# Kernel tuning notes

Hardware: AMD Instinct MI355X
Metric: run time of the kernel (lower is better)

Reference implementation:

```python
import jax, jax.numpy as jnp
import numpy as np

B, H, S, D = 8, 12, 1024, 64

def setup_inputs() -> dict:
    key = jax.random.key(0)
    kq, kk, kv = jax.random.split(key, 3)
    q = jax.random.normal(kq, (B, H, S, D), dtype=jnp.float32)
    k = jax.random.normal(kk, (B, H, S, D), dtype=jnp.float32)
    v = jax.random.normal(kv, (B, H, S, D), dtype=jnp.float32)
    scale = 8  # sqrt(d_head)
    return {"q": q, "k": k, "v": v, "scale": scale}

def reference(q, k, v, scale):
    # scores: (B,H,S,S) = q @ k^T / scale, softmax over last axis
    scores = jnp.einsum('bhqd,bhkd->bhqk', q, k) / scale
    attention_score = jax.nn.softmax(scores, axis=-1)
    # context: (B,H,S,D)
    attention_context = jnp.einsum('bhqk,bhkd->bhqd', attention_score, v)
    return (attention_score, attention_context)
```

## Files before the change

kernel.cpp:

```cpp
#include <hip/hip_runtime.h>


#define SLEN 1024
#define DHEAD 64
#define NBH 96
#define QROWS 16

typedef __attribute__((ext_vector_type(4))) float f32x4;
typedef __attribute__((ext_vector_type(8))) __bf16 bf16x8;

#define PL_STRIDE 1032

struct SMem {
  __bf16 pl[QROWS][PL_STRIDE];
  __bf16 qt[QROWS][72];
  float red[8][QROWS];
  float mrow[QROWS];
  float invrow[QROWS];
  float ctxr[4][64][4];
};

__global__ __launch_bounds__(512, 4)
void attn_fused(const float* __restrict__ Qp, const float* __restrict__ Kp,
                const float* __restrict__ Vp, const int* __restrict__ scale_p,
                float* __restrict__ out) {
  __shared__ SMem sm;
  const int tid  = threadIdx.x;
  const int w    = tid >> 6;
  const int lane = tid & 63;
  const int quad = lane >> 4;
  const int c16  = lane & 15;

  const int bid  = blockIdx.x;
  const int xcd  = bid & 7;
  const int slot = bid >> 3;
  const int bh   = xcd * 12 + (slot >> 6);
  const int qbase = (slot & 63) * QROWS;

  int siv = *scale_p;
  float fs = (siv >= 1 && siv <= (1 << 24)) ? (float)siv : __int_as_float(siv);
  const float inv_scale = 1.0f / fs;

  const float* Qg = Qp + ((size_t)bh * SLEN + qbase) * DHEAD;
  const float* Kg = Kp + (size_t)bh * SLEN * DHEAD;
  const float* Vg = Vp + (size_t)bh * SLEN * DHEAD;

  if (tid < 256) {
    int r = tid >> 4, d = (tid & 15) * 4;
    f32x4 qv = *(const f32x4*)(Qg + (size_t)r * DHEAD + d);
    #pragma unroll
    for (int j = 0; j < 4; ++j) sm.qt[r][d + j] = (__bf16)(qv[j] * inv_scale);
  }
  __syncthreads();

  bf16x8 af[2];
  #pragma unroll
  for (int k0 = 0; k0 < 2; ++k0)
    af[k0] = *(const bf16x8*)&sm.qt[c16][k0 * 32 + quad * 8];

  f32x4 acc[8];
  {
    f32x4 z = {0.0f, 0.0f, 0.0f, 0.0f};
    #pragma unroll
    for (int ct = 0; ct < 8; ++ct) acc[ct] = z;
  }

  #pragma unroll
  for (int ct = 0; ct < 8; ++ct) {
    int krow = w * 128 + ct * 16 + c16;
    const float* kr = Kg + (size_t)krow * DHEAD + quad * 8;
    f32x4 k0a = *(const f32x4*)(kr);
    f32x4 k0b = *(const f32x4*)(kr + 4);
    f32x4 k1a = *(const f32x4*)(kr + 32);
    f32x4 k1b = *(const f32x4*)(kr + 36);
    bf16x8 b0, b1;
    #pragma unroll
    for (int j = 0; j < 4; ++j) {
      b0[j]     = (__bf16)k0a[j];
      b0[j + 4] = (__bf16)k0b[j];
      b1[j]     = (__bf16)k1a[j];
      b1[j + 4] = (__bf16)k1b[j];
    }
    acc[ct] = __builtin_amdgcn_mfma_f32_16x16x32_bf16(af[0], b0, acc[ct], 0, 0, 0);
    acc[ct] = __builtin_amdgcn_mfma_f32_16x16x32_bf16(af[1], b1, acc[ct], 0, 0, 0);
  }

  float mx[4];
  #pragma unroll
  for (int i = 0; i < 4; ++i) {
    float m = acc[0][i];
    #pragma unroll
    for (int ct = 1; ct < 8; ++ct) m = fmaxf(m, acc[ct][i]);
    mx[i] = m;
  }
  #pragma unroll
  for (int off = 1; off < 16; off <<= 1)
    #pragma unroll
    for (int i = 0; i < 4; ++i)
      mx[i] = fmaxf(mx[i], __shfl_xor(mx[i], off));
  if (c16 == 0) {
    #pragma unroll
    for (int i = 0; i < 4; ++i) sm.red[w][quad * 4 + i] = mx[i];
  }
  __syncthreads();
  if (tid < QROWS) {
    float m = sm.red[0][tid];
    #pragma unroll
    for (int w2 = 1; w2 < 8; ++w2) m = fmaxf(m, sm.red[w2][tid]);
    sm.mrow[tid] = m;
  }
  __syncthreads();

  float sum4[4];
  #pragma unroll
  for (int i = 0; i < 4; ++i) {
    float m = sm.mrow[quad * 4 + i];
    float s = 0.0f;
    #pragma unroll
    for (int ct = 0; ct < 8; ++ct) {
      float e = __expf(acc[ct][i] - m);
      acc[ct][i] = e;
      s += e;
    }
    sum4[i] = s;
  }
  #pragma unroll
  for (int off = 1; off < 16; off <<= 1)
    #pragma unroll
    for (int i = 0; i < 4; ++i)
      sum4[i] += __shfl_xor(sum4[i], off);
  if (c16 == 0) {
    #pragma unroll
    for (int i = 0; i < 4; ++i) sm.red[w][quad * 4 + i] = sum4[i];
  }
  __syncthreads();
  if (tid < QROWS) {
    float s = 0.0f;
    #pragma unroll
    for (int w2 = 0; w2 < 8; ++w2) s += sm.red[w2][tid];
    sm.invrow[tid] = 1.0f / s;
  }
  __syncthreads();

  #pragma unroll
  for (int i = 0; i < 4; ++i) {
    int row = quad * 4 + i;
    float inv = sm.invrow[row];
    bf16x8 pk;
    #pragma unroll
    for (int ct = 0; ct < 8; ++ct) {
      float p = acc[ct][i] * inv;
      acc[ct][i] = p;
      pk[ct] = (__bf16)p;
    }
    *(bf16x8*)&sm.pl[row][w * 128 + c16 * 8] = pk;
  }
  __syncthreads();

  const int kpar = w >> 2;
  const int dt   = w & 3;
  const float* Vb = Vg + dt * 16 + c16;

  f32x4 ctx = {0.0f, 0.0f, 0.0f, 0.0f};
  float vr0[8], vr1[8];
  bf16x8 pa0, pa1;

  auto ldv = [&](float (&dst)[8], int itl) {
    int kb = (kpar * 4 + (itl >> 2)) * 128 + (itl & 3) * 4 + quad;
    #pragma unroll
    for (int j = 0; j < 8; ++j)
      dst[j] = Vb[(size_t)((kb + j * 16) * DHEAD)];
  };
  auto lda = [&](bf16x8& d, int itl) {
    d = *(const bf16x8*)&sm.pl[c16][(kpar * 4 + (itl >> 2)) * 128 +
                                    (itl & 3) * 32 + quad * 8];
  };

  ldv(vr0, 0); lda(pa0, 0);
  #pragma unroll
  for (int it = 0; it < 16; it += 2) {
    ldv(vr1, it + 1); lda(pa1, it + 1);
    bf16x8 bf0;
    #pragma unroll
    for (int j = 0; j < 8; ++j) bf0[j] = (__bf16)vr0[j];
    ctx = __builtin_amdgcn_mfma_f32_16x16x32_bf16(pa0, bf0, ctx, 0, 0, 0);
    if (it + 2 < 16) { ldv(vr0, it + 2); lda(pa0, it + 2); }
    bf16x8 bf1;
    #pragma unroll
    for (int j = 0; j < 8; ++j) bf1[j] = (__bf16)vr1[j];
    ctx = __builtin_amdgcn_mfma_f32_16x16x32_bf16(pa1, bf1, ctx, 0, 0, 0);
  }

  if (kpar == 1) *(f32x4*)&sm.ctxr[dt][lane][0] = ctx;
  __syncthreads();
  if (kpar == 0) {
    f32x4 o = *(const f32x4*)&sm.ctxr[dt][lane][0];
    float* outC = out + (size_t)NBH * SLEN * SLEN;
    #pragma unroll
    for (int i = 0; i < 4; ++i) {
      float r = ctx[i] + o[i];
      outC[((size_t)bh * SLEN + qbase + quad * 4 + i) * DHEAD + dt * 16 + c16] = r;
    }
  }

  #pragma unroll
  for (int i = 0; i < 4; ++i) {
    int row = quad * 4 + i;
    float* orow = out + ((size_t)bh * SLEN + qbase + row) * SLEN;
    #pragma unroll
    for (int ct = 0; ct < 8; ++ct)
      orow[w * 128 + ct * 16 + c16] = acc[ct][i];
  }
}

extern "C" void kernel_launch(void* const* d_in, const int* in_sizes, int n_in,
                              void* d_out, int out_size, void* d_ws, size_t ws_size,
                              hipStream_t stream) {
  (void)in_sizes; (void)n_in; (void)d_ws; (void)ws_size; (void)out_size;
  const float* q = (const float*)d_in[0];
  const float* k = (const float*)d_in[1];
  const float* v = (const float*)d_in[2];
  const int* scale = (const int*)d_in[3];
  float* out = (float*)d_out;
  dim3 grid((SLEN / QROWS) * NBH);
  dim3 block(512);
  hipLaunchKernelGGL(attn_fused, grid, block, 0, stream, q, k, v, scale, out);
}
```

Before: 693.5 us.

## Pre-convert K and transposed V to bf16 in workspace, restructure main kernel

Adds a prepass kernel that converts K to bf16 and V to a transposed bf16 layout in the workspace, so the main kernel reads half the bytes and gets contiguous V loads instead of strided scalar gathers. The main kernel drops to 256 threads with 4 waves each covering 256 keys. It computes K·Q^T so each lane owns a query column, writes the probabilities directly as f32x4 from registers without the LDS P buffer, and reduces partial contexts through LDS. It costs an extra launch and a workspace round-trip per call, and falls back to an unstaged path when the workspace is too small.

```diff
diff --git a/kernel.cpp b/kernel.cpp
--- a/kernel.cpp
+++ b/kernel.cpp
@@ -7,23 +7,67 @@
 #define QROWS 16
 
 typedef __attribute__((ext_vector_type(4))) float f32x4;
+typedef __attribute__((ext_vector_type(4))) __bf16 bf16x4;
 typedef __attribute__((ext_vector_type(8))) __bf16 bf16x8;
 
-#define PL_STRIDE 1032
+union BF8 { bf16x8 v; bf16x4 h[2]; };
+
+#define KB_ELEMS ((size_t)NBH * SLEN * DHEAD)
+#define WS_BYTES (KB_ELEMS * 2 * 2)
+
+__global__ __launch_bounds__(256)
+void prepass(const float* __restrict__ Kp, const float* __restrict__ Vp,
+             __bf16* __restrict__ Kb, __bf16* __restrict__ VTb) {
+  __shared__ float tf[64][68];
+  const int b = blockIdx.x, t = threadIdx.x;
+  if (b < 1536) {
+    const int bh = b >> 4, kc = b & 15;
+    const float* Vg = Vp + ((size_t)bh * SLEN + (size_t)kc * 64) * DHEAD;
+    #pragma unroll
+    for (int i = 0; i < 4; ++i) {
+      int r = i * 16 + (t >> 4), d0 = (t & 15) * 4;
+      f32x4 v = *(const f32x4*)(Vg + (size_t)r * DHEAD + d0);
+      #pragma unroll
+      for (int j = 0; j < 4; ++j) tf[r][d0 + j] = v[j];
+    }
+    __syncthreads();
+    const int d = t >> 2, k0 = (t & 3) * 16;
+    __bf16* dst = VTb + ((size_t)bh * DHEAD + d) * SLEN + kc * 64 + k0;
+    BF8 o0, o1;
+    #pragma unroll
+    for (int kk = 0; kk < 8; ++kk) {
+      o0.v[kk] = (__bf16)tf[k0 + kk][d];
+      o1.v[kk] = (__bf16)tf[k0 + 8 + kk][d];
+    }
+    *(bf16x8*)dst = o0.v;
+    *(bf16x8*)(dst + 8) = o1.v;
+  } else {
+    const size_t base = (size_t)(b - 1536) * 4096;
+    #pragma unroll
+    for (int i = 0; i < 4; ++i) {
+      size_t off = base + i * 1024 + t * 4;
+      f32x4 v = *(const f32x4*)(Kp + off);
+      bf16x4 o;
+      #pragma unroll
+      for (int j = 0; j < 4; ++j) o[j] = (__bf16)v[j];
+      *(bf16x4*)(Kb + off) = o;
+    }
+  }
+}
 
 struct SMem {
-  __bf16 pl[QROWS][PL_STRIDE];
-  __bf16 qt[QROWS][72];
-  float red[8][QROWS];
-  float mrow[QROWS];
-  float invrow[QROWS];
-  float ctxr[4][64][4];
+  __bf16 qt[QROWS][80];
+  float red_m[4][16];
+  float red_s[4][16];
+  float ctxr[4][QROWS][72];
 };
 
-__global__ __launch_bounds__(512, 4)
-void attn_fused(const float* __restrict__ Qp, const float* __restrict__ Kp,
-                const float* __restrict__ Vp, const int* __restrict__ scale_p,
-                float* __restrict__ out) {
+template<bool STAGED>
+__global__ __launch_bounds__(256, 4)
+void attn_main(const float* __restrict__ Qp, const float* __restrict__ Kp,
+               const float* __restrict__ Vp, const __bf16* __restrict__ Kb,
+               const __bf16* __restrict__ VTb, const int* __restrict__ scale_p,
+               float* __restrict__ out) {
   __shared__ SMem sm;
   const int tid  = threadIdx.x;
   const int w    = tid >> 6;
@@ -31,198 +75,172 @@
   const int quad = lane >> 4;
   const int c16  = lane & 15;
 
-  const int bid  = blockIdx.x;
-  const int xcd  = bid & 7;
-  const int slot = bid >> 3;
-  const int bh   = xcd * 12 + (slot >> 6);
+  const int bid   = blockIdx.x;
+  const int slot  = bid >> 3;
+  const int bh    = (bid & 7) * 12 + (slot >> 6);
   const int qbase = (slot & 63) * QROWS;
 
   int siv = *scale_p;
   float fs = (siv >= 1 && siv <= (1 << 24)) ? (float)siv : __int_as_float(siv);
   const float inv_scale = 1.0f / fs;
 
-  const float* Qg = Qp + ((size_t)bh * SLEN + qbase) * DHEAD;
-  const float* Kg = Kp + (size_t)bh * SLEN * DHEAD;
-  const float* Vg = Vp + (size_t)bh * SLEN * DHEAD;
-
-  if (tid < 256) {
-    int r = tid >> 4, d = (tid & 15) * 4;
-    f32x4 qv = *(const f32x4*)(Qg + (size_t)r * DHEAD + d);
-    #pragma unroll
-    for (int j = 0; j < 4; ++j) sm.qt[r][d + j] = (__bf16)(qv[j] * inv_scale);
-  }
-  __syncthreads();
-
-  bf16x8 af[2];
-  #pragma unroll
-  for (int k0 = 0; k0 < 2; ++k0)
-    af[k0] = *(const bf16x8*)&sm.qt[c16][k0 * 32 + quad * 8];
-
-  f32x4 acc[8];
+  {
+    int r = tid >> 4, d0 = (tid & 15) * 4;
+    f32x4 qv = *(const f32x4*)(Qp + ((size_t)bh * SLEN + qbase + r) * DHEAD + d0);
+    bf16x4 o;
+    #pragma unroll
+    for (int j = 0; j < 4; ++j) o[j] = (__bf16)(qv[j] * inv_scale);
+    *(bf16x4*)&sm.qt[r][d0] = o;
+  }
+  __syncthreads();
+
+  BF8 qf0, qf1;
+  qf0.v = *(const bf16x8*)&sm.qt[c16][quad * 8];
+  qf1.v = *(const bf16x8*)&sm.qt[c16][32 + quad * 8];
+
+  f32x4 acc[16];
   {
     f32x4 z = {0.0f, 0.0f, 0.0f, 0.0f};
     #pragma unroll
-    for (int ct = 0; ct < 8; ++ct) acc[ct] = z;
-  }
-
-  #pragma unroll
-  for (int ct = 0; ct < 8; ++ct) {
-    int krow = w * 128 + ct * 16 + c16;
-    const float* kr = Kg + (size_t)krow * DHEAD + quad * 8;
-    f32x4 k0a = *(const f32x4*)(kr);
-    f32x4 k0b = *(const f32x4*)(kr + 4);
-    f32x4 k1a = *(const f32x4*)(kr + 32);
-    f32x4 k1b = *(const f32x4*)(kr + 36);
-    bf16x8 b0, b1;
+    for (int mt = 0; mt < 16; ++mt) acc[mt] = z;
+  }
+  const __bf16* Kbbase = STAGED ? Kb + ((size_t)bh * SLEN + w * 256) * DHEAD : nullptr;
+  const float*  Kfbase = Kp + ((size_t)bh * SLEN + (size_t)w * 256) * DHEAD;
+  #pragma unroll
+  for (int mt = 0; mt < 16; ++mt) {
+    int row = mt * 16 + c16;
+    bf16x8 a0, a1;
+    if constexpr (STAGED) {
+      a0 = *(const bf16x8*)(Kbbase + (size_t)row * DHEAD + quad * 8);
+      a1 = *(const bf16x8*)(Kbbase + (size_t)row * DHEAD + 32 + quad * 8);
+    } else {
+      const float* kr = Kfbase + (size_t)row * DHEAD + quad * 8;
+      f32x4 x0 = *(const f32x4*)(kr);
+      f32x4 x1 = *(const f32x4*)(kr + 4);
+      f32x4 y0 = *(const f32x4*)(kr + 32);
+      f32x4 y1 = *(const f32x4*)(kr + 36);
+      #pragma unroll
+      for (int j = 0; j < 4; ++j) {
+        a0[j] = (__bf16)x0[j]; a0[j + 4] = (__bf16)x1[j];
+        a1[j] = (__bf16)y0[j]; a1[j + 4] = (__bf16)y1[j];
+      }
+    }
+    acc[mt] = __builtin_amdgcn_mfma_f32_16x16x32_bf16(a0, qf0.v, acc[mt], 0, 0, 0);
+    acc[mt] = __builtin_amdgcn_mfma_f32_16x16x32_bf16(a1, qf1.v, acc[mt], 0, 0, 0);
+  }
+
+  float m;
+  {
+    float a = fmaxf(fmaxf(acc[0][0], acc[0][1]), fmaxf(acc[0][2], acc[0][3]));
+    #pragma unroll
+    for (int mt = 1; mt < 16; ++mt) {
+      float b2 = fmaxf(fmaxf(acc[mt][0], acc[mt][1]), fmaxf(acc[mt][2], acc[mt][3]));
+      a = fmaxf(a, b2);
+    }
+    a = fmaxf(a, __shfl_xor(a, 16));
+    a = fmaxf(a, __shfl_xor(a, 32));
+    if (lane < 16) sm.red_m[w][c16] = a;
+  }
+  __syncthreads();
+  m = fmaxf(fmaxf(sm.red_m[0][c16], sm.red_m[1][c16]),
+            fmaxf(sm.red_m[2][c16], sm.red_m[3][c16]));
+
+  float s = 0.0f;
+  #pragma unroll
+  for (int mt = 0; mt < 16; ++mt)
     #pragma unroll
     for (int j = 0; j < 4; ++j) {
-      b0[j]     = (__bf16)k0a[j];
-      b0[j + 4] = (__bf16)k0b[j];
-      b1[j]     = (__bf16)k1a[j];
-      b1[j + 4] = (__bf16)k1b[j];
-    }
-    acc[ct] = __builtin_amdgcn_mfma_f32_16x16x32_bf16(af[0], b0, acc[ct], 0, 0, 0);
-    acc[ct] = __builtin_amdgcn_mfma_f32_16x16x32_bf16(af[1], b1, acc[ct], 0, 0, 0);
-  }
-
-  float mx[4];
-  #pragma unroll
-  for (int i = 0; i < 4; ++i) {
-    float m = acc[0][i];
-    #pragma unroll
-    for (int ct = 1; ct < 8; ++ct) m = fmaxf(m, acc[ct][i]);
-    mx[i] = m;
-  }
-  #pragma unroll
-  for (int off = 1; off < 16; off <<= 1)
+      float e = __expf(acc[mt][j] - m);
+      acc[mt][j] = e;
+      s += e;
+    }
+  s += __shfl_xor(s, 16);
+  s += __shfl_xor(s, 32);
+  if (lane < 16) sm.red_s[w][c16] = s;
+  __syncthreads();
+  const float inv = 1.0f / (sm.red_s[0][c16] + sm.red_s[1][c16] +
+                            sm.red_s[2][c16] + sm.red_s[3][c16]);
+
+  float* orow = out + ((size_t)bh * SLEN + qbase + c16) * SLEN + w * 256;
+  BF8 pf[8];
+  #pragma unroll
+  for (int mt = 0; mt < 16; ++mt) {
+    f32x4 p;
+    #pragma unroll
+    for (int j = 0; j < 4; ++j) p[j] = acc[mt][j] * inv;
+    *(f32x4*)(orow + mt * 16 + quad * 4) = p;
+    #pragma unroll
+    for (int j = 0; j < 4; ++j)
+      pf[mt >> 1].v[(mt & 1) * 4 + j] = (__bf16)p[j];
+  }
+
+  f32x4 ctx[4];
+  {
+    f32x4 z = {0.0f, 0.0f, 0.0f, 0.0f};
+    #pragma unroll
+    for (int dt = 0; dt < 4; ++dt) ctx[dt] = z;
+  }
+  const __bf16* Vt = STAGED ? VTb + (size_t)bh * DHEAD * SLEN : nullptr;
+  #pragma unroll
+  for (int t8 = 0; t8 < 8; ++t8) {
+    int k0 = w * 256 + t8 * 32 + quad * 4;
+    #pragma unroll
+    for (int dt = 0; dt < 4; ++dt) {
+      BF8 b;
+      if constexpr (STAGED) {
+        const __bf16* vr = Vt + (size_t)(dt * 16 + c16) * SLEN + k0;
+        b.h[0] = *(const bf16x4*)(vr);
+        b.h[1] = *(const bf16x4*)(vr + 16);
+      } else {
+        #pragma unroll
+        for (int j = 0; j < 8; ++j)
+          b.v[j] = (__bf16)Vp[((size_t)bh * SLEN + k0 + (j & 3) + 16 * (j >> 2)) * DHEAD +
+                              dt * 16 + c16];
+      }
+      ctx[dt] = __builtin_amdgcn_mfma_f32_16x16x32_bf16(pf[t8].v, b.v, ctx[dt], 0, 0, 0);
+    }
+  }
+
+  #pragma unroll
+  for (int dt = 0; dt < 4; ++dt)
     #pragma unroll
     for (int i = 0; i < 4; ++i)
-      mx[i] = fmaxf(mx[i], __shfl_xor(mx[i], off));
-  if (c16 == 0) {
-    #pragma unroll
-    for (int i = 0; i < 4; ++i) sm.red[w][quad * 4 + i] = mx[i];
-  }
-  __syncthreads();
-  if (tid < QROWS) {
-    float m = sm.red[0][tid];
-    #pragma unroll
-    for (int w2 = 1; w2 < 8; ++w2) m = fmaxf(m, sm.red[w2][tid]);
-    sm.mrow[tid] = m;
-  }
-  __syncthreads();
-
-  float sum4[4];
-  #pragma unroll
-  for (int i = 0; i < 4; ++i) {
-    float m = sm.mrow[quad * 4 + i];
-    float s = 0.0f;
-    #pragma unroll
-    for (int ct = 0; ct < 8; ++ct) {
-      float e = __expf(acc[ct][i] - m);
-      acc[ct][i] = e;
-      s += e;
-    }
-    sum4[i] = s;
-  }
-  #pragma unroll
-  for (int off = 1; off < 16; off <<= 1)
-    #pragma unroll
-    for (int i = 0; i < 4; ++i)
-      sum4[i] += __shfl_xor(sum4[i], off);
-  if (c16 == 0) {
-    #pragma unroll
-    for (int i = 0; i < 4; ++i) sm.red[w][quad * 4 + i] = sum4[i];
-  }
-  __syncthreads();
-  if (tid < QROWS) {
-    float s = 0.0f;
-    #pragma unroll
-    for (int w2 = 0; w2 < 8; ++w2) s += sm.red[w2][tid];
-    sm.invrow[tid] = 1.0f / s;
-  }
-  __syncthreads();
-
-  #pragma unroll
-  for (int i = 0; i < 4; ++i) {
-    int row = quad * 4 + i;
-    float inv = sm.invrow[row];
-    bf16x8 pk;
-    #pragma unroll
-    for (int ct = 0; ct < 8; ++ct) {
-      float p = acc[ct][i] * inv;
-      acc[ct][i] = p;
-      pk[ct] = (__bf16)p;
-    }
-    *(bf16x8*)&sm.pl[row][w * 128 + c16 * 8] = pk;
-  }
-  __syncthreads();
-
-  const int kpar = w >> 2;
-  const int dt   = w & 3;
-  const float* Vb = Vg + dt * 16 + c16;
-
-  f32x4 ctx = {0.0f, 0.0f, 0.0f, 0.0f};
-  float vr0[8], vr1[8];
-  bf16x8 pa0, pa1;
-
-  auto ldv = [&](float (&dst)[8], int itl) {
-    int kb = (kpar * 4 + (itl >> 2)) * 128 + (itl & 3) * 4 + quad;
-    #pragma unroll
-    for (int j = 0; j < 8; ++j)
-      dst[j] = Vb[(size_t)((kb + j * 16) * DHEAD)];
-  };
-  auto lda = [&](bf16x8& d, int itl) {
-    d = *(const bf16x8*)&sm.pl[c16][(kpar * 4 + (itl >> 2)) * 128 +
-                                    (itl & 3) * 32 + quad * 8];
-  };
-
-  ldv(vr0, 0); lda(pa0, 0);
-  #pragma unroll
-  for (int it = 0; it < 16; it += 2) {
-    ldv(vr1, it + 1); lda(pa1, it + 1);
-    bf16x8 bf0;
-    #pragma unroll
-    for (int j = 0; j < 8; ++j) bf0[j] = (__bf16)vr0[j];
-    ctx = __builtin_amdgcn_mfma_f32_16x16x32_bf16(pa0, bf0, ctx, 0, 0, 0);
-    if (it + 2 < 16) { ldv(vr0, it + 2); lda(pa0, it + 2); }
-    bf16x8 bf1;
-    #pragma unroll
-    for (int j = 0; j < 8; ++j) bf1[j] = (__bf16)vr1[j];
-    ctx = __builtin_amdgcn_mfma_f32_16x16x32_bf16(pa1, bf1, ctx, 0, 0, 0);
-  }
-
-  if (kpar == 1) *(f32x4*)&sm.ctxr[dt][lane][0] = ctx;
-  __syncthreads();
-  if (kpar == 0) {
-    f32x4 o = *(const f32x4*)&sm.ctxr[dt][lane][0];
+      sm.ctxr[w][quad * 4 + i][dt * 16 + c16] = ctx[dt][i];
+  __syncthreads();
+  {
+    int q = tid >> 4, d4 = (tid & 15) * 4;
+    f32x4 r0 = *(const f32x4*)&sm.ctxr[0][q][d4];
+    f32x4 r1 = *(const f32x4*)&sm.ctxr[1][q][d4];
+    f32x4 r2 = *(const f32x4*)&sm.ctxr[2][q][d4];
+    f32x4 r3 = *(const f32x4*)&sm.ctxr[3][q][d4];
+    f32x4 o;
+    #pragma unroll
+    for (int j = 0; j < 4; ++j) o[j] = (r0[j] + r1[j]) + (r2[j] + r3[j]);
     float* outC = out + (size_t)NBH * SLEN * SLEN;
-    #pragma unroll
-    for (int i = 0; i < 4; ++i) {
-      float r = ctx[i] + o[i];
-      outC[((size_t)bh * SLEN + qbase + quad * 4 + i) * DHEAD + dt * 16 + c16] = r;
-    }
-  }
-
-  #pragma unroll
-  for (int i = 0; i < 4; ++i) {
-    int row = quad * 4 + i;
-    float* orow = out + ((size_t)bh * SLEN + qbase + row) * SLEN;
-    #pragma unroll
-    for (int ct = 0; ct < 8; ++ct)
-      orow[w * 128 + ct * 16 + c16] = acc[ct][i];
+    *(f32x4*)(outC + ((size_t)bh * SLEN + qbase + q) * DHEAD + d4) = o;
   }
 }
 
 extern "C" void kernel_launch(void* const* d_in, const int* in_sizes, int n_in,
                               void* d_out, int out_size, void* d_ws, size_t ws_size,
                               hipStream_t stream) {
-  (void)in_sizes; (void)n_in; (void)d_ws; (void)ws_size; (void)out_size;
+  (void)in_sizes; (void)n_in; (void)out_size;
   const float* q = (const float*)d_in[0];
   const float* k = (const float*)d_in[1];
   const float* v = (const float*)d_in[2];
   const int* scale = (const int*)d_in[3];
   float* out = (float*)d_out;
-  dim3 grid((SLEN / QROWS) * NBH);
-  dim3 block(512);
-  hipLaunchKernelGGL(attn_fused, grid, block, 0, stream, q, k, v, scale, out);
+
+  const bool staged = (d_ws != nullptr) && (ws_size >= (size_t)WS_BYTES);
+  dim3 block(256);
+  if (staged) {
+    __bf16* Kb  = (__bf16*)d_ws;
+    __bf16* VTb = Kb + KB_ELEMS;
+    hipLaunchKernelGGL(prepass, dim3(3072), block, 0, stream, k, v, Kb, VTb);
+    hipLaunchKernelGGL(attn_main<true>, dim3((SLEN / QROWS) * NBH), block, 0, stream,
+                       q, k, v, Kb, VTb, scale, out);
+  } else {
+    hipLaunchKernelGGL(attn_main<false>, dim3((SLEN / QROWS) * NBH), block, 0, stream,
+                       q, k, v, (const __bf16*)nullptr, (const __bf16*)nullptr, scale, out);
+  }
 }
```

Result: slower. 718.7 us (+3.6%).
